# Performance work log

Hardware: AMD Instinct MI355X
Metric: run time of the kernel (lower is better)

## Reference

```python
import jax, jax.numpy as jnp
import numpy as np
from jax import lax

PADDING_L = 30  # causal: kernel_size - 1


def setup_inputs() -> dict:
    key = jax.random.key(0)
    k1, k2 = jax.random.split(key)
    T, B, C = 4096, 8, 1024
    H, K = 16, 31
    x = jax.random.normal(k1, (T, B, C), dtype=jnp.float32)
    weight = jax.random.normal(k2, (H, K), dtype=jnp.float32)
    return {"x": x, "weight": weight}


def reference(x, weight):
    # x: [T, B, C]; weight: [H, K]
    T, B, C = x.shape
    H, K = weight.shape
    R = C // H  # channels per head share the same kernel
    # weight_softmax=True: normalize kernel taps per head
    w = jax.nn.softmax(weight, axis=-1)            # [H, K]
    wc = jnp.repeat(w, R, axis=0)[:, None, :]      # [C, 1, K] depthwise kernel
    xb = jnp.transpose(x, (1, 2, 0))               # [B, C, T]
    # lightconv_cuda: out[b,c,t] = sum_k w[h(c),k] * x_pad[b,c,t+k],
    # left pad = padding_l, right pad = K-1-padding_l (cross-correlation)
    out = lax.conv_general_dilated(
        xb, wc,
        window_strides=(1,),
        padding=[(PADDING_L, K - 1 - PADDING_L)],
        feature_group_count=C,
        dimension_numbers=("NCH", "OIH", "NCH"),
    )                                              # [B, C, T]
    return jnp.transpose(out, (2, 0, 1))           # [T, B, C]
```

## Files before the change

kernel.cpp:

```cpp
#include <hip/hip_runtime.h>
#include <math.h>

#define T_DIM 4096
#define B_DIM 8
#define C_DIM 1024
#define H_DIM 16
#define K_DIM 31
#define PAD_L 30
#define TILE_T 32
#define WIN 62
#define BLOCK 256
#define RING_ROWS 64
#define TPB 8

typedef __attribute__((ext_vector_type(4))) float f32x4;

__device__ __forceinline__ void stage16(const float* g, float* l) {
    __builtin_amdgcn_global_load_lds(
        (const __attribute__((address_space(1))) void*)g,
        (__attribute__((address_space(3))) void*)l,
        16, 0, 0);
}


template <int TPAR, int J>
__device__ __forceinline__ void conv_a(const float* col,
                                       const float (&taps)[K_DIM],
                                       float (&acc)[TILE_T]) {
    if constexpr (J < 30) {
        const float xj = col[((TPAR + J + 34) & 63) * BLOCK];
        #pragma unroll
        for (int i = 0; i <= J; ++i) {
            if (i == J) acc[i] = taps[0] * xj;
            else        acc[i] = fmaf(taps[J - i], xj, acc[i]);
        }
        conv_a<TPAR, J + 1>(col, taps, acc);
    }
}

template <int TPAR, int J>
__device__ __forceinline__ void conv_b(const float* col,
                                       const float (&taps)[K_DIM],
                                       float (&acc)[TILE_T],
                                       float* po, long stride) {
    if constexpr (J < WIN) {
        const float xj = col[((TPAR + J + 34) & 63) * BLOCK];
        constexpr int ilo = J - 30;
        constexpr int ihi = (J < TILE_T - 1) ? J : TILE_T - 1;
        #pragma unroll
        for (int i = ilo; i <= ihi; ++i) {
            if (i == J) acc[i] = taps[0] * xj;
            else        acc[i] = fmaf(taps[J - i], xj, acc[i]);
        }
        __builtin_nontemporal_store(acc[J - 30], po + (long)(J - 30) * stride);
        conv_b<TPAR, J + 1>(col, taps, acc, po, stride);
    }
}

template <int TPAR>
__device__ __forceinline__ void iter_body(
    const float* __restrict__ x, float* __restrict__ out,
    const float* col, float* lds0,
    const float (&taps)[K_DIM],
    long t0, int wv, int lane, int cc0, int tid, bool stage_next)
{
    const long stride = (long)B_DIM * C_DIM;
    float acc[TILE_T];

    conv_a<TPAR, 0>(col, taps, acc);

    __syncthreads();

    if (stage_next) {
        const long g0 = t0 + TILE_T + wv * 8;
        const float* gp = x + g0 * stride + cc0 + lane * 4;
        float* lp = lds0 + ((TPAR + TILE_T + wv * 8) & 63) * BLOCK;
        #pragma unroll
        for (int i = 0; i < 8; ++i)
            stage16(gp + (long)i * stride, lp + i * BLOCK);
    }

    float* po = out + t0 * stride + cc0 + tid;
    conv_b<TPAR, 30>(col, taps, acc, po, stride);

    __syncthreads();
}

__global__ __launch_bounds__(BLOCK, 2) void lightconv_kernel(
    const float* __restrict__ x,
    const float* __restrict__ w,
    float* __restrict__ out)
{
    __shared__ float ring[RING_ROWS][BLOCK];

    const int tid    = threadIdx.x;
    const int lane   = tid & 63;
    const int wv     = tid >> 6;
    const int colBlk = blockIdx.x;
    const int tg     = blockIdx.y;
    const int cc0    = colBlk * BLOCK;
    const long stride = (long)B_DIM * C_DIM;
    const long tgbase = (long)tg * (TPB * TILE_T);

    {
        const int r0 = wv * 16;
        const int rn = (wv == 3) ? 14 : 16;
        #pragma unroll
        for (int i = 0; i < 16; ++i) {
            if (i < rn) {
                const long gr = tgbase - PAD_L + r0 + i;
                const int slot = ((int)gr) & 63;
                if (gr >= 0) {
                    stage16(x + gr * stride + cc0 + lane * 4, &ring[slot][0]);
                } else {
                    const f32x4 z = {0.f, 0.f, 0.f, 0.f};
                    *(f32x4*)&ring[slot][lane * 4] = z;
                }
            }
        }
    }

    float taps[K_DIM];
    {
        const float* wr = w + (((colBlk & 3) << 2) + wv) * K_DIM;
        float tv[K_DIM];
        float m = -1e30f;
        #pragma unroll
        for (int k = 0; k < K_DIM; ++k) { tv[k] = wr[k]; m = fmaxf(m, tv[k]); }
        float s = 0.f;
        #pragma unroll
        for (int k = 0; k < K_DIM; ++k) { tv[k] = __expf(tv[k] - m); s += tv[k]; }
        const float inv = 1.0f / s;
        #pragma unroll
        for (int k = 0; k < K_DIM; ++k)
            taps[k] = __int_as_float(__builtin_amdgcn_readfirstlane(
                          __float_as_int(tv[k] * inv)));
    }

    __syncthreads();

    const float* col = &ring[0][0] + tid;
    float* lds0 = &ring[0][0];
    long t0 = tgbase;
    #pragma unroll 1
    for (int it = 0; it < TPB; ++it, t0 += TILE_T) {
        const bool sn = (it < TPB - 1);
        if (it & 1) iter_body<32>(x, out, col, lds0, taps, t0, wv, lane, cc0, tid, sn);
        else        iter_body< 0>(x, out, col, lds0, taps, t0, wv, lane, cc0, tid, sn);
    }
}

extern "C" void kernel_launch(void* const* d_in, const int* in_sizes, int n_in,
                              void* d_out, int out_size, void* d_ws, size_t ws_size,
                              hipStream_t stream) {
    const float* x = (const float*)d_in[0];
    const float* w = (const float*)d_in[1];
    float* out = (float*)d_out;

    dim3 grid((B_DIM * C_DIM) / BLOCK, T_DIM / (TPB * TILE_T));
    lightconv_kernel<<<grid, BLOCK, 0, stream>>>(x, w, out);
}
```

Baseline: 237.4 us.

## Shrink blocks to a single wavefront and replace barriers with waitcnt

Each block is now a single 64-lane wavefront covering 64 channels instead of 256. The LDS ring is restaged with a 16x4 lane layout, so each row is loaded with 16-byte async global-to-LDS loads spread across lanes. Because only one wave touches the ring, __syncthreads is replaced by explicit s_waitcnt instructions, which removes block barriers and lets the prefetch for the next tile overlap the current one. In exchange the grid has four times as many small blocks with a lower LDS footprint each, and correctness now depends on the hand-written vmcnt counts matching the number of outstanding loads.

```diff
diff --git a/kernel.cpp b/kernel.cpp
--- a/kernel.cpp
+++ b/kernel.cpp
@@ -9,8 +9,9 @@
 #define PAD_L 30
 #define TILE_T 32
 #define WIN 62
-#define BLOCK 256
-#define RING_ROWS 64
+#define BLOCK 64
+#define COLS 64
+#define RING 64
 #define TPB 8
 
 typedef __attribute__((ext_vector_type(4))) float f32x4;
@@ -22,13 +23,12 @@
         16, 0, 0);
 }
 
-
 template <int TPAR, int J>
 __device__ __forceinline__ void conv_a(const float* col,
                                        const float (&taps)[K_DIM],
                                        float (&acc)[TILE_T]) {
     if constexpr (J < 30) {
-        const float xj = col[((TPAR + J + 34) & 63) * BLOCK];
+        const float xj = col[((TPAR + J + 34) & 63) * COLS];
         #pragma unroll
         for (int i = 0; i <= J; ++i) {
             if (i == J) acc[i] = taps[0] * xj;
@@ -44,7 +44,7 @@
                                        float (&acc)[TILE_T],
                                        float* po, long stride) {
     if constexpr (J < WIN) {
-        const float xj = col[((TPAR + J + 34) & 63) * BLOCK];
+        const float xj = col[((TPAR + J + 34) & 63) * COLS];
         constexpr int ilo = J - 30;
         constexpr int ihi = (J < TILE_T - 1) ? J : TILE_T - 1;
         #pragma unroll
@@ -60,30 +60,27 @@
 template <int TPAR>
 __device__ __forceinline__ void iter_body(
     const float* __restrict__ x, float* __restrict__ out,
-    const float* col, float* lds0,
-    const float (&taps)[K_DIM],
-    long t0, int wv, int lane, int cc0, int tid, bool stage_next)
+    const float* col, float* lds0, const float (&taps)[K_DIM],
+    long t0, int c0, int lane, int lrow, int lcol, bool stage_next)
 {
     const long stride = (long)B_DIM * C_DIM;
     float acc[TILE_T];
 
     conv_a<TPAR, 0>(col, taps, acc);
 
-    __syncthreads();
+    asm volatile("s_waitcnt vmcnt(32) lgkmcnt(0)" ::: "memory");
 
     if (stage_next) {
-        const long g0 = t0 + TILE_T + wv * 8;
-        const float* gp = x + g0 * stride + cc0 + lane * 4;
-        float* lp = lds0 + ((TPAR + TILE_T + wv * 8) & 63) * BLOCK;
+        const float* gp = x + (t0 + TILE_T + lrow) * stride + c0 + lcol;
         #pragma unroll
-        for (int i = 0; i < 8; ++i)
-            stage16(gp + (long)i * stride, lp + i * BLOCK);
+        for (int g = 0; g < 8; ++g) {
+            const int slot = (TPAR + TILE_T + 4 * g) & 63;
+            stage16(gp + (long)(4 * g) * stride, lds0 + slot * COLS);
+        }
     }
 
-    float* po = out + t0 * stride + cc0 + tid;
+    float* po = out + t0 * stride + c0 + lane;
     conv_b<TPAR, 30>(col, taps, acc, po, stride);
-
-    __syncthreads();
 }
 
 __global__ __launch_bounds__(BLOCK, 2) void lightconv_kernel(
@@ -91,38 +88,43 @@
     const float* __restrict__ w,
     float* __restrict__ out)
 {
-    __shared__ float ring[RING_ROWS][BLOCK];
+    __shared__ float ring[RING][COLS];
 
-    const int tid    = threadIdx.x;
-    const int lane   = tid & 63;
-    const int wv     = tid >> 6;
+    const int lane   = threadIdx.x;
     const int colBlk = blockIdx.x;
     const int tg     = blockIdx.y;
-    const int cc0    = colBlk * BLOCK;
+    const int c0     = colBlk * COLS;
     const long stride = (long)B_DIM * C_DIM;
     const long tgbase = (long)tg * (TPB * TILE_T);
 
+    const int lrow = lane >> 4;
+    const int lcol = (lane & 15) << 2;
+
     {
-        const int r0 = wv * 16;
-        const int rn = (wv == 3) ? 14 : 16;
-        #pragma unroll
-        for (int i = 0; i < 16; ++i) {
-            if (i < rn) {
-                const long gr = tgbase - PAD_L + r0 + i;
-                const int slot = ((int)gr) & 63;
-                if (gr >= 0) {
-                    stage16(x + gr * stride + cc0 + lane * 4, &ring[slot][0]);
-                } else {
-                    const f32x4 z = {0.f, 0.f, 0.f, 0.f};
-                    *(f32x4*)&ring[slot][lane * 4] = z;
-                }
+        const float* gp = x + (tgbase - 32 + lrow) * stride + c0 + lcol;
+        if (tg > 0) {
+            #pragma unroll
+            for (int g = 0; g < 16; ++g) {
+                const int slot = (32 + 4 * g) & 63;
+                stage16(gp + (long)(4 * g) * stride, &ring[slot][0]);
+            }
+        } else {
+            #pragma unroll
+            for (int g = 0; g < 8; ++g) {
+                const int slot = 32 + 4 * g;
+                *(f32x4*)(&ring[slot][0] + lane * 4) = (f32x4){0.f, 0.f, 0.f, 0.f};
+            }
+            #pragma unroll
+            for (int g = 8; g < 16; ++g) {
+                const int slot = (32 + 4 * g) & 63;
+                stage16(gp + (long)(4 * g) * stride, &ring[slot][0]);
             }
         }
     }
 
     float taps[K_DIM];
     {
-        const float* wr = w + (((colBlk & 3) << 2) + wv) * K_DIM;
+        const float* wr = w + (colBlk & 15) * K_DIM;
         float tv[K_DIM];
         float m = -1e30f;
         #pragma unroll
@@ -137,16 +139,16 @@
                           __float_as_int(tv[k] * inv)));
     }
 
-    __syncthreads();
+    asm volatile("s_waitcnt vmcnt(0)" ::: "memory");
 
-    const float* col = &ring[0][0] + tid;
+    const float* col = &ring[0][0] + lane;
     float* lds0 = &ring[0][0];
     long t0 = tgbase;
     #pragma unroll 1
-    for (int it = 0; it < TPB; ++it, t0 += TILE_T) {
-        const bool sn = (it < TPB - 1);
-        if (it & 1) iter_body<32>(x, out, col, lds0, taps, t0, wv, lane, cc0, tid, sn);
-        else        iter_body< 0>(x, out, col, lds0, taps, t0, wv, lane, cc0, tid, sn);
+    for (int k = 0; k < TPB; ++k, t0 += TILE_T) {
+        const bool sn = (k < TPB - 1);
+        if (k & 1) iter_body<32>(x, out, col, lds0, taps, t0, c0, lane, lrow, lcol, sn);
+        else       iter_body< 0>(x, out, col, lds0, taps, t0, c0, lane, lrow, lcol, sn);
     }
 }
 
@@ -157,6 +159,6 @@
     const float* w = (const float*)d_in[1];
     float* out = (float*)d_out;
 
-    dim3 grid((B_DIM * C_DIM) / BLOCK, T_DIM / (TPB * TILE_T));
+    dim3 grid((B_DIM * C_DIM) / COLS, T_DIM / (TPB * TILE_T));
     lightconv_kernel<<<grid, BLOCK, 0, stream>>>(x, w, out);
 }
```

After: 246.1 us. 3.7% more time.
